# Optimization experiments

Measured on AMD Instinct MI355X. Metric: run time of the kernel, lower is better.

The kernel has to match this reference:

```python
import jax, jax.numpy as jnp
import numpy as np

B, S, E = 16, 2048, 1024

def setup_inputs() -> dict:
    key = jax.random.key(0)
    ks = jax.random.split(key, 7)
    scale = 1.0 / np.sqrt(E)
    x = jax.random.normal(ks[0], (B, S, E), dtype=jnp.float32)
    wq = jax.random.normal(ks[1], (E, E), dtype=jnp.float32) * scale
    bq = jax.random.normal(ks[2], (E,), dtype=jnp.float32) * 0.01
    wk = jax.random.normal(ks[3], (E, E), dtype=jnp.float32) * scale
    bk = jax.random.normal(ks[4], (E,), dtype=jnp.float32) * 0.01
    wv = jax.random.normal(ks[5], (E, E), dtype=jnp.float32) * scale
    bv = jax.random.normal(ks[6], (E,), dtype=jnp.float32) * 0.01
    return {"x": x, "wq": wq, "bq": bq, "wk": wk, "bk": bk, "wv": wv, "bv": bv}

def reference(x, wq, bq, wk, bk, wv, bv):
    # Linear layers: y = x @ W^T + b (torch nn.Linear convention)
    Q = jnp.einsum('bse,fe->bsf', x, wq) + bq
    K = jnp.einsum('bse,fe->bsf', x, wk) + bk
    V = jnp.einsum('bse,fe->bsf', x, wv) + bv
    scale = 1.0 / jnp.sqrt(jnp.asarray(x.shape[-1], dtype=x.dtype))
    score = jnp.einsum('bqe,bke->bqk', Q, K) * scale  # [B,S,S]
    attn = jax.nn.softmax(score, axis=-1)
    # dropout is identity in eval mode
    context = jnp.einsum('bqk,bke->bqe', attn, V)  # [B,S,E]
    return jnp.mean(context, axis=1)  # [B,E]
```

## Files before the change

### kernel.cpp

```cpp
#include <hip/hip_runtime.h>


#define B_ 16
#define S_ 2048
#define E_ 1024

typedef __bf16 bf16x8 __attribute__((ext_vector_type(8)));
typedef float f32x4 __attribute__((ext_vector_type(4)));
typedef float f32x2 __attribute__((ext_vector_type(2)));

__device__ __forceinline__ unsigned short f2bf(float f) {
  unsigned int u = __float_as_uint(f);
  u = (u + 0x7FFFu + ((u >> 16) & 1u)) >> 16;
  return (unsigned short)u;
}

__global__ __launch_bounds__(256) void gvec_kernel(
    const float* __restrict__ wk, const float* __restrict__ bq,
    float* __restrict__ g) {
  const int e = blockIdx.x * 256 + threadIdx.x;
  const int f0 = blockIdx.y * 32;
  float acc = 0.f;
#pragma unroll
  for (int i = 0; i < 32; ++i) acc += wk[(size_t)(f0 + i) * E_ + e] * bq[f0 + i];
  atomicAdd(&g[e], acc);
}

__global__ __launch_bounds__(256) void cast_x_v_kernel(
    const float* __restrict__ x, const float* __restrict__ g,
    unsigned short* __restrict__ xbf, float* __restrict__ vs) {
  const int row = blockIdx.x, t = threadIdx.x;
  const size_t i = (size_t)row * E_ + t * 4;
  float4 v = *(const float4*)(x + i);
  float4 gv = *(const float4*)(g + t * 4);
  ushort4 o;
  o.x = f2bf(v.x); o.y = f2bf(v.y); o.z = f2bf(v.z); o.w = f2bf(v.w);
  *(ushort4*)(xbf + i) = o;
  float p = v.x * gv.x + v.y * gv.y + v.z * gv.z + v.w * gv.w;
#pragma unroll
  for (int off = 32; off >= 1; off >>= 1) p += __shfl_xor(p, off);
  __shared__ float wsp[4];
  if ((t & 63) == 0) wsp[t >> 6] = p;
  __syncthreads();
  if (t == 0) vs[row] = (wsp[0] + wsp[1] + wsp[2] + wsp[3]) * 0.03125f;
}

__global__ __launch_bounds__(256) void tcast_kernel(
    const float* __restrict__ src, unsigned short* __restrict__ dst) {
  __shared__ float tile[32][33];
  const int tx = threadIdx.x & 31, ty = threadIdx.x >> 5;
  const int f0 = blockIdx.y * 32, e0 = blockIdx.x * 32;
#pragma unroll
  for (int j = 0; j < 4; ++j)
    tile[ty + 8 * j][tx] = src[(size_t)(f0 + ty + 8 * j) * E_ + e0 + tx];
  __syncthreads();
#pragma unroll
  for (int j = 0; j < 4; ++j)
    dst[(size_t)(e0 + ty + 8 * j) * E_ + f0 + tx] = f2bf(tile[tx][ty + 8 * j]);
}

template <int MODE>
__global__ __launch_bounds__(256, 2) void gemm_bt(
    const unsigned short* __restrict__ A, const unsigned short* __restrict__ Bm,
    void* __restrict__ Cout, const float* __restrict__ vs,
    float* __restrict__ rowsum, float scale,
    int K, int lda, int ldb, int ldc,
    long long strideA, long long strideB, long long strideC) {
  __shared__ unsigned short As[128 * 64];
  __shared__ unsigned short Bs[128 * 64];

  const int tid = threadIdx.x;
  const int wave = tid >> 6;
  const int lane = tid & 63;
  const int bz = blockIdx.z;
  const unsigned short* Ab = A + (size_t)bz * strideA;
  const unsigned short* Bb = Bm + (size_t)bz * strideB;
  const int rowBase = blockIdx.y * 128;
  const int colBase = blockIdx.x * 128;

  const int waveM = wave >> 1, waveN = wave & 1;
  const int lrow = lane & 15, lq = lane >> 4;

  const int rsub = lane >> 3;
  const int gOff = (((lane & 7) ^ rsub) << 3);

  f32x4 acc[4][4];
#pragma unroll
  for (int i = 0; i < 4; ++i)
#pragma unroll
    for (int j = 0; j < 4; ++j) {
      f32x4 z = {0.f, 0.f, 0.f, 0.f};
      acc[i][j] = z;
    }

  for (int k0 = 0; k0 < K; k0 += 64) {
#pragma unroll
    for (int i = 0; i < 4; ++i) {
      const int chunk = wave * 4 + i;
      const int r = chunk * 8 + rsub;
      const unsigned short* ga = Ab + (size_t)(rowBase + r) * lda + (k0 + gOff);
      const unsigned short* gb = Bb + (size_t)(colBase + r) * ldb + (k0 + gOff);
      __builtin_amdgcn_global_load_lds(
          (const __attribute__((address_space(1))) void*)ga,
          (__attribute__((address_space(3))) void*)(&As[chunk * 512]), 16, 0, 0);
      __builtin_amdgcn_global_load_lds(
          (const __attribute__((address_space(1))) void*)gb,
          (__attribute__((address_space(3))) void*)(&Bs[chunk * 512]), 16, 0, 0);
    }
    __syncthreads();

#pragma unroll
    for (int ks = 0; ks < 2; ++ks) {
      const int gg = (((ks * 4 + lq) ^ (lrow & 7)) << 3);
      bf16x8 af[4], bfv[4];
#pragma unroll
      for (int mi = 0; mi < 4; ++mi)
        af[mi] = *(const bf16x8*)(&As[(waveM * 64 + mi * 16 + lrow) * 64 + gg]);
#pragma unroll
      for (int ni = 0; ni < 4; ++ni)
        bfv[ni] = *(const bf16x8*)(&Bs[(waveN * 64 + ni * 16 + lrow) * 64 + gg]);
#pragma unroll
      for (int mi = 0; mi < 4; ++mi)
#pragma unroll
        for (int ni = 0; ni < 4; ++ni)
          acc[mi][ni] = __builtin_amdgcn_mfma_f32_16x16x32_bf16(
              af[mi], bfv[ni], acc[mi][ni], 0, 0, 0);
    }
    __syncthreads();
  }

  if constexpr (MODE == 0) {
    unsigned short* Cb = (unsigned short*)Cout;
#pragma unroll
    for (int mi = 0; mi < 4; ++mi) {
      const int grow = rowBase + waveM * 64 + mi * 16 + lq * 4;
#pragma unroll
      for (int ni = 0; ni < 4; ++ni) {
        const int gcol = colBase + waveN * 64 + ni * 16 + lrow;
#pragma unroll
        for (int r = 0; r < 4; ++r)
          Cb[(size_t)(grow + r) * ldc + gcol] = f2bf(acc[mi][ni][r]);
      }
    }
  } else {
    unsigned char* Eb = (unsigned char*)Cout + (size_t)bz * strideC;
    float* rs = rowsum + (size_t)bz * S_;
    const float* vsb = vs + (size_t)bz * S_;
    float badd[4];
#pragma unroll
    for (int ni = 0; ni < 4; ++ni)
      badd[ni] = vsb[colBase + waveN * 64 + ni * 16 + lrow];
#pragma unroll
    for (int mi = 0; mi < 4; ++mi) {
      const int grow = rowBase + waveM * 64 + mi * 16 + lq * 4;
#pragma unroll
      for (int r = 0; r < 4; ++r) {
        float e[4];
        float partial = 0.f;
#pragma unroll
        for (int ni = 0; ni < 4; ++ni) {
          e[ni] = __expf(acc[mi][ni][r] * scale + badd[ni]);
          partial += e[ni];
        }
        unsigned int pk = 0;
        pk = __builtin_amdgcn_cvt_pk_fp8_f32(e[0], e[1], pk, false);
        pk = __builtin_amdgcn_cvt_pk_fp8_f32(e[2], e[3], pk, true);
        *(unsigned int*)(&Eb[(size_t)(grow + r) * S_ + colBase + waveN * 64 +
                             lrow * 4]) = pk;
        partial += __shfl_xor(partial, 1);
        partial += __shfl_xor(partial, 2);
        partial += __shfl_xor(partial, 4);
        partial += __shfl_xor(partial, 8);
        if (lrow == 0) atomicAdd(&rs[grow + r], partial);
      }
    }
  }
}

__global__ __launch_bounds__(256) void colsum_kernel(
    const unsigned int* __restrict__ Epk, const float* __restrict__ rowsum,
    float* __restrict__ wsum) {
  const int b = blockIdx.y, q0 = blockIdx.x * 64, t = threadIdx.x;
  __shared__ float rinv[64];
  if (t < 64) rinv[t] = 1.0f / rowsum[(size_t)b * S_ + q0 + t];
  __syncthreads();
  float cs[2][4] = {{0, 0, 0, 0}, {0, 0, 0, 0}};
  const unsigned int* Eb = Epk + ((size_t)b * S_ + q0) * (S_ / 4);
  for (int q = 0; q < 64; ++q) {
    const float rv = rinv[q];
    const unsigned int* row = Eb + (size_t)q * (S_ / 4);
#pragma unroll
    for (int j = 0; j < 2; ++j) {
      const unsigned int p = row[t + 256 * j];
      f32x2 lo = __builtin_amdgcn_cvt_pk_f32_fp8(p, false);
      f32x2 hi = __builtin_amdgcn_cvt_pk_f32_fp8(p, true);
      cs[j][0] += lo[0] * rv;
      cs[j][1] += lo[1] * rv;
      cs[j][2] += hi[0] * rv;
      cs[j][3] += hi[1] * rv;
    }
  }
  const float inv = 1.0f / (float)S_;
#pragma unroll
  for (int j = 0; j < 2; ++j) {
    const int d = t + 256 * j;
    const int base = (d >> 4) * 64 + (d & 15);
#pragma unroll
    for (int jj = 0; jj < 4; ++jj)
      atomicAdd(&wsum[(size_t)b * S_ + base + 16 * jj], cs[j][jj] * inv);
  }
}

__global__ __launch_bounds__(256) void xbar_kernel(
    const unsigned short* __restrict__ xbf, const float* __restrict__ wsum,
    float* __restrict__ xbar) {
  const int b = blockIdx.y, kc = blockIdx.x, t = threadIdx.x;
  float4 acc = {0.f, 0.f, 0.f, 0.f};
  for (int k0 = 0; k0 < 128; ++k0) {
    const int k = kc * 128 + k0;
    const float w = wsum[(size_t)b * S_ + k];
    const ushort4 xv =
        *(const ushort4*)(xbf + ((size_t)b * S_ + k) * E_ + t * 4);
    acc.x += w * __uint_as_float((unsigned int)xv.x << 16);
    acc.y += w * __uint_as_float((unsigned int)xv.y << 16);
    acc.z += w * __uint_as_float((unsigned int)xv.z << 16);
    acc.w += w * __uint_as_float((unsigned int)xv.w << 16);
  }
  float* xb = xbar + (size_t)b * E_ + t * 4;
  atomicAdd(&xb[0], acc.x);
  atomicAdd(&xb[1], acc.y);
  atomicAdd(&xb[2], acc.z);
  atomicAdd(&xb[3], acc.w);
}

__global__ __launch_bounds__(256) void out_kernel(
    const float* __restrict__ xbar, const float* __restrict__ wv,
    const float* __restrict__ bv, float* __restrict__ out) {
  const int gid = blockIdx.x * 256 + threadIdx.x;
  const int b = gid >> 10, e = gid & 1023;
  const int c0 = blockIdx.y * 64;
  const float4* xr = (const float4*)(xbar + (size_t)b * E_) + c0;
  const float4* wr = (const float4*)(wv + (size_t)e * E_) + c0;
  float s = 0.f;
  for (int j = 0; j < 64; ++j) {
    float4 a = xr[j], w = wr[j];
    s += a.x * w.x + a.y * w.y + a.z * w.z + a.w * w.w;
  }
  if (blockIdx.y == 0) s += bv[e];
  atomicAdd(&out[gid], s);
}

extern "C" void kernel_launch(void* const* d_in, const int* in_sizes, int n_in,
                              void* d_out, int out_size, void* d_ws,
                              size_t ws_size, hipStream_t stream) {
  const float* x = (const float*)d_in[0];
  const float* wq = (const float*)d_in[1];
  const float* bq = (const float*)d_in[2];
  const float* wk = (const float*)d_in[3];
  const float* wv = (const float*)d_in[5];
  const float* bv = (const float*)d_in[6];
  float* out = (float*)d_out;

  char* ws = (char*)d_ws;
  const size_t MB = 1ull << 20;
  unsigned short* xbf = (unsigned short*)(ws);
  unsigned short* y = (unsigned short*)(ws + 64 * MB);
  unsigned char* Ebuf = (unsigned char*)(ws + 128 * MB);
  unsigned short* WqT = (unsigned short*)(ws + 192 * MB);
  unsigned short* WkT = (unsigned short*)(ws + 194 * MB);
  unsigned short* Mt = (unsigned short*)(ws + 196 * MB);
  float* g = (float*)(ws + 198 * MB);
  float* rowsum = g + E_;
  float* wsum = rowsum + B_ * S_;
  float* xbar = wsum + B_ * S_;
  float* vs = xbar + B_ * E_;

  hipMemsetAsync(g, 0, (size_t)(E_ + 2 * B_ * S_ + B_ * E_) * sizeof(float),
                 stream);
  hipMemsetAsync(out, 0, (size_t)B_ * E_ * sizeof(float), stream);

  gvec_kernel<<<dim3(E_ / 256, 32), 256, 0, stream>>>(wk, bq, g);
  cast_x_v_kernel<<<B_ * S_, 256, 0, stream>>>(x, g, xbf, vs);
  tcast_kernel<<<dim3(32, 32), 256, 0, stream>>>(wq, WqT);
  tcast_kernel<<<dim3(32, 32), 256, 0, stream>>>(wk, WkT);

  gemm_bt<0><<<dim3(8, 8), 256, 0, stream>>>(
      WkT, WqT, (void*)Mt, nullptr, nullptr, 1.0f, E_, E_, E_, E_, 0, 0, 0);
  gemm_bt<0><<<dim3(E_ / 128, (B_ * S_) / 128), 256, 0, stream>>>(
      xbf, Mt, (void*)y, nullptr, nullptr, 1.0f, E_, E_, E_, E_, 0, 0, 0);
  gemm_bt<1><<<dim3(S_ / 128, S_ / 128, B_), 256, 0, stream>>>(
      y, xbf, (void*)Ebuf, vs, rowsum, 0.03125f, E_, E_, E_, S_,
      (long long)S_ * E_, (long long)S_ * E_, (long long)S_ * S_);

  colsum_kernel<<<dim3(S_ / 64, B_), 256, 0, stream>>>(
      (const unsigned int*)Ebuf, rowsum, wsum);
  xbar_kernel<<<dim3(16, B_), 256, 0, stream>>>(xbf, wsum, xbar);
  out_kernel<<<dim3(B_ * E_ / 256, 4), 256, 0, stream>>>(xbar, wv, bv, out);
}
```

Measured before the change: 490.9 us.

## Remap GEMM workgroups across XCDs and retune reduction kernel grids

The GEMM kernel now remaps its linear block index so that consecutive tiles land on the same XCD (stride-8 interleave), which should improve L2 reuse on the chiplet GPU. The cast kernel processes one row per wave instead of one row per block, which removes the shared-memory reduction and the barrier. The colsum and xbar kernels halve their per-block work and double their grids to expose more parallelism, and they add unroll pragmas. The extra grids raise the number of atomic adds. The remap assumes the block count is divisible by 8.

Result: no change. 497.9 us (+1.4%).

```diff
diff --git a/kernel.cpp b/kernel.cpp
--- a/kernel.cpp
+++ b/kernel.cpp
@@ -29,20 +29,26 @@
 __global__ __launch_bounds__(256) void cast_x_v_kernel(
     const float* __restrict__ x, const float* __restrict__ g,
     unsigned short* __restrict__ xbf, float* __restrict__ vs) {
-  const int row = blockIdx.x, t = threadIdx.x;
-  const size_t i = (size_t)row * E_ + t * 4;
-  float4 v = *(const float4*)(x + i);
-  float4 gv = *(const float4*)(g + t * 4);
-  ushort4 o;
-  o.x = f2bf(v.x); o.y = f2bf(v.y); o.z = f2bf(v.z); o.w = f2bf(v.w);
-  *(ushort4*)(xbf + i) = o;
-  float p = v.x * gv.x + v.y * gv.y + v.z * gv.z + v.w * gv.w;
+  const int t = threadIdx.x;
+  const int row = blockIdx.x * 4 + (t >> 6);
+  const int lane = t & 63;
+  const float4* xr = (const float4*)(x + (size_t)row * E_);
+  const float4* g4 = (const float4*)g;
+  ushort4* xb4 = (ushort4*)(xbf + (size_t)row * E_);
+  float p = 0.f;
+#pragma unroll
+  for (int j = 0; j < 4; ++j) {
+    const int idx = j * 64 + lane;
+    float4 v = xr[idx];
+    float4 gv = g4[idx];
+    ushort4 o;
+    o.x = f2bf(v.x); o.y = f2bf(v.y); o.z = f2bf(v.z); o.w = f2bf(v.w);
+    xb4[idx] = o;
+    p += v.x * gv.x + v.y * gv.y + v.z * gv.z + v.w * gv.w;
+  }
 #pragma unroll
   for (int off = 32; off >= 1; off >>= 1) p += __shfl_xor(p, off);
-  __shared__ float wsp[4];
-  if ((t & 63) == 0) wsp[t >> 6] = p;
-  __syncthreads();
-  if (t == 0) vs[row] = (wsp[0] + wsp[1] + wsp[2] + wsp[3]) * 0.03125f;
+  if (lane == 0) vs[row] = p * 0.03125f;
 }
 
 __global__ __launch_bounds__(256) void tcast_kernel(
@@ -72,11 +78,21 @@
   const int tid = threadIdx.x;
   const int wave = tid >> 6;
   const int lane = tid & 63;
-  const int bz = blockIdx.z;
+
+  const unsigned nwg = gridDim.x * gridDim.y * gridDim.z;
+  const unsigned lin =
+      blockIdx.x + gridDim.x * (blockIdx.y + gridDim.y * blockIdx.z);
+  const unsigned cpx = nwg >> 3;
+  const unsigned tz = (lin & 7) * cpx + (lin >> 3);
+  const unsigned bxi = tz % gridDim.x;
+  const unsigned rest = tz / gridDim.x;
+  const unsigned byi = rest % gridDim.y;
+  const unsigned bz = rest / gridDim.y;
+
   const unsigned short* Ab = A + (size_t)bz * strideA;
   const unsigned short* Bb = Bm + (size_t)bz * strideB;
-  const int rowBase = blockIdx.y * 128;
-  const int colBase = blockIdx.x * 128;
+  const int rowBase = byi * 128;
+  const int colBase = bxi * 128;
 
   const int waveM = wave >> 1, waveN = wave & 1;
   const int lrow = lane & 15, lq = lane >> 4;
@@ -180,13 +196,14 @@
 __global__ __launch_bounds__(256) void colsum_kernel(
     const unsigned int* __restrict__ Epk, const float* __restrict__ rowsum,
     float* __restrict__ wsum) {
-  const int b = blockIdx.y, q0 = blockIdx.x * 64, t = threadIdx.x;
-  __shared__ float rinv[64];
-  if (t < 64) rinv[t] = 1.0f / rowsum[(size_t)b * S_ + q0 + t];
+  const int b = blockIdx.y, q0 = blockIdx.x * 32, t = threadIdx.x;
+  __shared__ float rinv[32];
+  if (t < 32) rinv[t] = 1.0f / rowsum[(size_t)b * S_ + q0 + t];
   __syncthreads();
   float cs[2][4] = {{0, 0, 0, 0}, {0, 0, 0, 0}};
   const unsigned int* Eb = Epk + ((size_t)b * S_ + q0) * (S_ / 4);
-  for (int q = 0; q < 64; ++q) {
+#pragma unroll 2
+  for (int q = 0; q < 32; ++q) {
     const float rv = rinv[q];
     const unsigned int* row = Eb + (size_t)q * (S_ / 4);
 #pragma unroll
@@ -216,8 +233,9 @@
     float* __restrict__ xbar) {
   const int b = blockIdx.y, kc = blockIdx.x, t = threadIdx.x;
   float4 acc = {0.f, 0.f, 0.f, 0.f};
-  for (int k0 = 0; k0 < 128; ++k0) {
-    const int k = kc * 128 + k0;
+#pragma unroll 4
+  for (int k0 = 0; k0 < 64; ++k0) {
+    const int k = kc * 64 + k0;
     const float w = wsum[(size_t)b * S_ + k];
     const ushort4 xv =
         *(const ushort4*)(xbf + ((size_t)b * S_ + k) * E_ + t * 4);
@@ -280,7 +298,7 @@
   hipMemsetAsync(out, 0, (size_t)B_ * E_ * sizeof(float), stream);
 
   gvec_kernel<<<dim3(E_ / 256, 32), 256, 0, stream>>>(wk, bq, g);
-  cast_x_v_kernel<<<B_ * S_, 256, 0, stream>>>(x, g, xbf, vs);
+  cast_x_v_kernel<<<B_ * S_ / 4, 256, 0, stream>>>(x, g, xbf, vs);
   tcast_kernel<<<dim3(32, 32), 256, 0, stream>>>(wq, WqT);
   tcast_kernel<<<dim3(32, 32), 256, 0, stream>>>(wk, WkT);
 
@@ -292,8 +310,8 @@
       y, xbf, (void*)Ebuf, vs, rowsum, 0.03125f, E_, E_, E_, S_,
       (long long)S_ * E_, (long long)S_ * E_, (long long)S_ * S_);
 
-  colsum_kernel<<<dim3(S_ / 64, B_), 256, 0, stream>>>(
+  colsum_kernel<<<dim3(S_ / 32, B_), 256, 0, stream>>>(
       (const unsigned int*)Ebuf, rowsum, wsum);
-  xbar_kernel<<<dim3(16, B_), 256, 0, stream>>>(xbf, wsum, xbar);
+  xbar_kernel<<<dim3(32, B_), 256, 0, stream>>>(xbf, wsum, xbar);
   out_kernel<<<dim3(B_ * E_ / 256, 4), 256, 0, stream>>>(xbar, wv, bv, out);
 }
```
